# Kernel optimization log

Hardware: AMD Instinct MI355X
Metric: run time of the kernel (lower is better)

Reference implementation:

```python
import jax, jax.numpy as jnp
import numpy as np

B, N, D, H = 8, 384, 256, 1024

def setup_inputs() -> dict:
    key = jax.random.key(0)
    ks = jax.random.split(key, 8)
    x = jax.random.normal(ks[0], (B, N, D), jnp.float32)
    adj = jnp.ones((B, N, N), jnp.float32)
    box_num = jax.random.randint(ks[1], (B, 1), 1, N + 1).astype(jnp.int64)
    box_num = box_num.at[0, 0].set(N)  # original code assumes max(box_num) == N
    fc1_w = jax.random.normal(ks[2], (H, D), jnp.float32) * (1.0 / np.sqrt(D))
    fc1_b = jnp.zeros((H,), jnp.float32)
    fc2_w = jax.random.normal(ks[3], (D, H), jnp.float32) * (1.0 / np.sqrt(H))
    fc2_b = jnp.zeros((D,), jnp.float32)
    learn_w = jax.random.uniform(ks[4], (D,), jnp.float32)  # uniform_(0,1) init
    return {"x": x, "adj": adj, "box_num": box_num,
            "fc1_w": fc1_w, "fc1_b": fc1_b, "fc2_w": fc2_w, "fc2_b": fc2_b,
            "learn_w": learn_w}

def reference(x, adj, box_num, fc1_w, fc1_b, fc2_w, fc2_b, learn_w):
    # mlp: fc2(relu(fc1(x)))  -> x_hat (B,N,D)
    x_hat = jnp.maximum(x @ fc1_w.T + fc1_b, 0.0) @ fc2_w.T + fc2_b
    # dynamic mask: -1 where either node i or j is padding, 0 otherwise
    valid = jnp.arange(N)[None, :] < box_num            # (B,N)
    pair_valid = valid[:, None, :] & valid[:, :, None]  # (B,N,N)
    mask = jnp.where(pair_valid, 0.0, -1.0)             # (B,N,N)
    # pairwise weighted L1 distance: einsum('bijd,d->bij', |x_i - x_j| + mask, w)
    # mask broadcasts over d, so its contribution is mask * sum(w) (same math,
    # avoids a second (B,N,N,D) materialization)
    absdiff = jnp.abs(x_hat[:, :, None, :] - x_hat[:, None, :, :])  # (B,N,N,D)
    dist = jnp.einsum('bijd,d->bij', absdiff, learn_w) + mask * jnp.sum(learn_w)
    out = jax.nn.leaky_relu(dist, negative_slope=0.01)
    out = out - jnp.max(out, axis=-1, keepdims=True)
    soft_adj = adj * jnp.exp(out)
    soft_adj = soft_adj / jnp.sum(soft_adj, axis=-1, keepdims=True) + 1e-10
    return soft_adj, x_hat
```

## Files before the change

kernel.cpp:

```cpp
#include <hip/hip_runtime.h>
#include <math.h>

#define B_ 8
#define N_ 384
#define D_ 256
#define H_ 1024

typedef __bf16 bh;
typedef __bf16 bh4   __attribute__((ext_vector_type(4)));
typedef __bf16 bf16x8 __attribute__((ext_vector_type(8)));
typedef float  f32x4  __attribute__((ext_vector_type(4)));
typedef _Float16 h2 __attribute__((ext_vector_type(2)));

#if __has_builtin(__builtin_amdgcn_fdot2)
#define FDOT2(a,b,c) __builtin_amdgcn_fdot2((a),(b),(c),false)
#else
#define FDOT2(a,b,c) ((c) + (float)(a).x*(float)(b).x + (float)(a).y*(float)(b).y)
#endif

#define GLDS16(gp, lp) __builtin_amdgcn_global_load_lds( \
    (const __attribute__((address_space(1))) unsigned*)(gp), \
    (__attribute__((address_space(3))) unsigned*)(lp), 16, 0, 0)

__device__ inline h2 habs2(h2 x) {
    unsigned u = __builtin_bit_cast(unsigned, x) & 0x7fff7fffu;
    return __builtin_bit_cast(h2, u);
}

__device__ inline void split2(float v, bh& h, bh& l) {
    h = (bh)v;
    l = (bh)(v - (float)h);
}

__device__ inline int load_boxnum(const int* __restrict__ p, int b) {
    bool is64 = ((p[1] | p[3] | p[5] | p[7]) == 0);
    return is64 ? p[2 * b] : p[b];
}

__global__ __launch_bounds__(256) void prep_split(
        const float* __restrict__ x, const float* __restrict__ w1, const float* __restrict__ w2,
        bh* __restrict__ xh, bh* __restrict__ xl,
        bh* __restrict__ w1h, bh* __restrict__ w1l,
        bh* __restrict__ w2h, bh* __restrict__ w2l) {
    const int blk = blockIdx.x;
    const float* src; bh *dh, *dl; int idx;
    if (blk < 768)       { src = x;  dh = xh;  dl = xl;  idx = blk * 256 + threadIdx.x; }
    else if (blk < 1024) { src = w1; dh = w1h; dl = w1l; idx = (blk - 768) * 256 + threadIdx.x; }
    else                 { src = w2; dh = w2h; dl = w2l; idx = (blk - 1024) * 256 + threadIdx.x; }
    float4 v = ((const float4*)src)[idx];
    float f[4] = {v.x, v.y, v.z, v.w};
    bh4 hv, lv;
    #pragma unroll
    for (int i = 0; i < 4; i++) { bh h, l; split2(f[i], h, l); hv[i] = h; lv[i] = l; }
    *(bh4*)&dh[4 * (size_t)idx] = hv;
    *(bh4*)&dl[4 * (size_t)idx] = lv;
}

__global__ __launch_bounds__(256) void gemm1_kernel(
        const bh* __restrict__ xh, const bh* __restrict__ xl,
        const bh* __restrict__ w1h, const bh* __restrict__ w1l,
        const float* __restrict__ bias,
        bh* __restrict__ c1h, bh* __restrict__ c1l) {
    __shared__ __align__(16) bh lds[16384];
    const int tid = threadIdx.x, lane = tid & 63, w = tid >> 6;
    const int m0 = blockIdx.y * 128, n0 = blockIdx.x * 128;
    const int lr = lane >> 2, kb = lane & 3;
    const int kbp = kb ^ ((lr >> 1) & 3);
    const bh* psrc; int rowbase;
    if (w == 0)      { psrc = xh;  rowbase = m0; }
    else if (w == 1) { psrc = xl;  rowbase = m0; }
    else if (w == 2) { psrc = w1h; rowbase = n0; }
    else             { psrc = w1l; rowbase = n0; }
    const bh* gsrc = psrc + (size_t)(rowbase + lr) * 256 + kbp * 8;
    bh* lwb = &lds[w * 4096 + lane * 8];
    const int l15 = lane & 15, q = lane >> 4;
    const int swq = q ^ ((l15 >> 1) & 3);
    const int wm = (w & 1) * 64, wn = (w >> 1) * 64;

    f32x4 acc[4][4] = {};
    for (int k0 = 0; k0 < 256; k0 += 32) {
        __syncthreads();
        #pragma unroll
        for (int s = 0; s < 8; s++)
            GLDS16(gsrc + (size_t)s * 4096 + k0, lwb + s * 512);
        __syncthreads();
        bf16x8 fa[4][2], fb[4][2];
        #pragma unroll
        for (int i = 0; i < 4; i++) {
            int ra = wm + i * 16 + l15;
            int rb = wn + i * 16 + l15;
            fa[i][0] = *(const bf16x8*)&lds[        ra * 32 + swq * 8];
            fa[i][1] = *(const bf16x8*)&lds[ 4096 + ra * 32 + swq * 8];
            fb[i][0] = *(const bf16x8*)&lds[ 8192 + rb * 32 + swq * 8];
            fb[i][1] = *(const bf16x8*)&lds[12288 + rb * 32 + swq * 8];
        }
        #pragma unroll
        for (int mi = 0; mi < 4; mi++)
            #pragma unroll
            for (int ni = 0; ni < 4; ni++) {
                acc[mi][ni] = __builtin_amdgcn_mfma_f32_16x16x32_bf16(fa[mi][0], fb[ni][0], acc[mi][ni], 0, 0, 0);
                acc[mi][ni] = __builtin_amdgcn_mfma_f32_16x16x32_bf16(fa[mi][0], fb[ni][1], acc[mi][ni], 0, 0, 0);
                acc[mi][ni] = __builtin_amdgcn_mfma_f32_16x16x32_bf16(fa[mi][1], fb[ni][0], acc[mi][ni], 0, 0, 0);
            }
    }
    #pragma unroll
    for (int ni = 0; ni < 4; ni++) {
        int col = n0 + wn + ni * 16 + l15;
        float bb = bias[col];
        #pragma unroll
        for (int mi = 0; mi < 4; mi++)
            #pragma unroll
            for (int reg = 0; reg < 4; reg++) {
                int row = m0 + wm + mi * 16 + q * 4 + reg;
                float v = fmaxf(acc[mi][ni][reg] + bb, 0.f);
                bh h, l; split2(v, h, l);
                size_t off = (size_t)row * H_ + col;
                c1h[off] = h; c1l[off] = l;
            }
    }
}

__global__ __launch_bounds__(256) void gemm2_kernel(
        const bh* __restrict__ c1h, const bh* __restrict__ c1l,
        const bh* __restrict__ w2h, const bh* __restrict__ w2l,
        const float* __restrict__ bias,
        float* __restrict__ C) {
    __shared__ __align__(16) bh lds[24576];
    const int tid = threadIdx.x, lane = tid & 63, w = tid >> 6;
    const int m0 = blockIdx.y * 64, n0 = blockIdx.x * 128;
    const int lr = lane >> 3, kb = lane & 7;
    const int kbp = kb ^ lr;
    const int l15 = lane & 15, q = lane >> 4;
    const int wn = w * 32;

    f32x4 acc[4][2] = {};
    for (int k0 = 0; k0 < 1024; k0 += 64) {
        __syncthreads();
        #pragma unroll
        for (int j = 0; j < 12; j++) {
            int c = w * 12 + j;
            const bh* g; int ldsbase, s;
            if (c < 8)       { g = c1h; ldsbase = 0;     s = c;      g += (size_t)(m0 + s * 8 + lr) * 1024; }
            else if (c < 16) { g = c1l; ldsbase = 4096;  s = c - 8;  g += (size_t)(m0 + s * 8 + lr) * 1024; }
            else if (c < 32) { g = w2h; ldsbase = 8192;  s = c - 16; g += (size_t)(n0 + s * 8 + lr) * 1024; }
            else             { g = w2l; ldsbase = 16384; s = c - 32; g += (size_t)(n0 + s * 8 + lr) * 1024; }
            GLDS16(g + k0 + kbp * 8, &lds[ldsbase + s * 512 + lane * 8]);
        }
        __syncthreads();
        #pragma unroll
        for (int ks = 0; ks < 2; ks++) {
            const int p = (ks * 4 + q) ^ (l15 & 7);
            bf16x8 fa[4][2], fb[2][2];
            #pragma unroll
            for (int mi = 0; mi < 4; mi++) {
                int ra = mi * 16 + l15;
                fa[mi][0] = *(const bf16x8*)&lds[       ra * 64 + p * 8];
                fa[mi][1] = *(const bf16x8*)&lds[4096 + ra * 64 + p * 8];
            }
            #pragma unroll
            for (int ni = 0; ni < 2; ni++) {
                int rb = wn + ni * 16 + l15;
                fb[ni][0] = *(const bf16x8*)&lds[ 8192 + rb * 64 + p * 8];
                fb[ni][1] = *(const bf16x8*)&lds[16384 + rb * 64 + p * 8];
            }
            #pragma unroll
            for (int mi = 0; mi < 4; mi++)
                #pragma unroll
                for (int ni = 0; ni < 2; ni++) {
                    acc[mi][ni] = __builtin_amdgcn_mfma_f32_16x16x32_bf16(fa[mi][0], fb[ni][0], acc[mi][ni], 0, 0, 0);
                    acc[mi][ni] = __builtin_amdgcn_mfma_f32_16x16x32_bf16(fa[mi][0], fb[ni][1], acc[mi][ni], 0, 0, 0);
                    acc[mi][ni] = __builtin_amdgcn_mfma_f32_16x16x32_bf16(fa[mi][1], fb[ni][0], acc[mi][ni], 0, 0, 0);
                }
        }
    }
    #pragma unroll
    for (int ni = 0; ni < 2; ni++) {
        int col = n0 + wn + ni * 16 + l15;
        float bb = bias[col];
        #pragma unroll
        for (int mi = 0; mi < 4; mi++)
            #pragma unroll
            for (int reg = 0; reg < 4; reg++) {
                int row = m0 + mi * 16 + q * 4 + reg;
                C[(size_t)row * D_ + col] = acc[mi][ni][reg] + bb;
            }
    }
}

#define DLP 68
__global__ __launch_bounds__(256) void dist_kernel(const float* __restrict__ xhat,
                                                   const float* __restrict__ w,
                                                   const int* __restrict__ box_num,
                                                   float* __restrict__ dist) {
    __shared__ __align__(16) unsigned XiU[16 * DLP];
    __shared__ __align__(16) unsigned XjU[16 * DLP];
    const int bidx = blockIdx.x;
    const int b = bidx / 21;
    int p = bidx % 21;
    int ti = 0;
    while (p >= 6 - ti) { p -= 6 - ti; ti++; }
    const int tj = ti + p;
    const int i0 = ti * 64, j0 = tj * 64;

    const int tid = threadIdx.x;
    const int tx = tid & 15, ty = tid >> 4;
    const int lane = tid & 63;
    const int r = tid >> 2, kq = (tid & 3) * 8;
    const int kq2 = (tid & 3) * 4;

    float sumw = w[lane] + w[lane + 64] + w[lane + 128] + w[lane + 192];
    #pragma unroll
    for (int off = 32; off > 0; off >>= 1) sumw += __shfl_xor(sumw, off);

    const float* xb = xhat + (size_t)b * N_ * D_;
    float acc[4][4] = {};

    for (int k0 = 0; k0 < D_; k0 += 32) {
        h2 wk2[16];
        #pragma unroll
        for (int c = 0; c < 16; c++) {
            float2 wp = *(const float2*)&w[k0 + 2 * c];
            wk2[c] = (h2){(_Float16)wp.x, (_Float16)wp.y};
        }
        const float* ip = xb + (size_t)(i0 + r) * D_ + k0 + kq;
        const float* jp = xb + (size_t)(j0 + r) * D_ + k0 + kq;
        float4 i0v = *(const float4*)ip, i1v = *(const float4*)(ip + 4);
        float4 j0v = *(const float4*)jp, j1v = *(const float4*)(jp + 4);
        float fi[8] = {i0v.x, i0v.y, i0v.z, i0v.w, i1v.x, i1v.y, i1v.z, i1v.w};
        float fj[8] = {j0v.x, j0v.y, j0v.z, j0v.w, j1v.x, j1v.y, j1v.z, j1v.w};
        __syncthreads();
        #pragma unroll
        for (int c = 0; c < 4; c++) {
            h2 hi = (h2){(_Float16)fi[2 * c], (_Float16)fi[2 * c + 1]};
            h2 hj = (h2){(_Float16)fj[2 * c], (_Float16)fj[2 * c + 1]};
            XiU[(kq2 + c) * DLP + r] = __builtin_bit_cast(unsigned, hi);
            XjU[(kq2 + c) * DLP + r] = __builtin_bit_cast(unsigned, hj);
        }
        __syncthreads();
        #pragma unroll
        for (int k2 = 0; k2 < 16; k2++) {
            uint4 ar = *(const uint4*)&XiU[k2 * DLP + ty * 4];
            uint4 br = *(const uint4*)&XjU[k2 * DLP + tx * 4];
            h2 ai[4] = {__builtin_bit_cast(h2, ar.x), __builtin_bit_cast(h2, ar.y),
                        __builtin_bit_cast(h2, ar.z), __builtin_bit_cast(h2, ar.w)};
            h2 bj[4] = {__builtin_bit_cast(h2, br.x), __builtin_bit_cast(h2, br.y),
                        __builtin_bit_cast(h2, br.z), __builtin_bit_cast(h2, br.w)};
            h2 wv = wk2[k2];
            #pragma unroll
            for (int ii = 0; ii < 4; ii++)
                #pragma unroll
                for (int jj = 0; jj < 4; jj++) {
                    h2 d = habs2(ai[ii] - bj[jj]);
                    acc[ii][jj] = FDOT2(d, wv, acc[ii][jj]);
                }
        }
    }

    const int bn = load_boxnum(box_num, b);
    float m[4][4];
    #pragma unroll
    for (int ii = 0; ii < 4; ii++) {
        int i = i0 + ty * 4 + ii;
        bool vi = i < bn;
        #pragma unroll
        for (int jj = 0; jj < 4; jj++) {
            int j = j0 + tx * 4 + jj;
            float v = acc[ii][jj];
            if (!(vi && (j < bn))) v -= sumw;
            m[ii][jj] = v > 0.f ? v : 0.01f * v;
        }
    }
    #pragma unroll
    for (int ii = 0; ii < 4; ii++) {
        int i = i0 + ty * 4 + ii;
        float4 o = {m[ii][0], m[ii][1], m[ii][2], m[ii][3]};
        *(float4*)&dist[((size_t)b * N_ + i) * N_ + j0 + tx * 4] = o;
    }
    #pragma unroll
    for (int jj = 0; jj < 4; jj++) {
        int j = j0 + tx * 4 + jj;
        float4 o = {m[0][jj], m[1][jj], m[2][jj], m[3][jj]};
        *(float4*)&dist[((size_t)b * N_ + j) * N_ + i0 + ty * 4] = o;
    }
}

__global__ __launch_bounds__(256) void softmax_kernel(float* __restrict__ sa,
                                                      const float* __restrict__ adj) {
    const int row = blockIdx.x * 4 + (threadIdx.x >> 6);
    const int t = threadIdx.x & 63;
    float* prow = sa + (size_t)row * N_;
    const float* arow = adj + (size_t)row * N_;
    float v[6];
    float m = -1e30f;
    #pragma unroll
    for (int qq = 0; qq < 6; qq++) { v[qq] = prow[t + qq * 64]; m = fmaxf(m, v[qq]); }
    #pragma unroll
    for (int off = 32; off > 0; off >>= 1) m = fmaxf(m, __shfl_xor(m, off));
    float e[6];
    float s = 0.f;
    #pragma unroll
    for (int qq = 0; qq < 6; qq++) { e[qq] = arow[t + qq * 64] * expf(v[qq] - m); s += e[qq]; }
    #pragma unroll
    for (int off = 32; off > 0; off >>= 1) s += __shfl_xor(s, off);
    float inv = 1.0f / s;
    #pragma unroll
    for (int qq = 0; qq < 6; qq++) prow[t + qq * 64] = e[qq] * inv + 1e-10f;
}

extern "C" void kernel_launch(void* const* d_in, const int* in_sizes, int n_in,
                              void* d_out, int out_size, void* d_ws, size_t ws_size,
                              hipStream_t stream) {
    const float* x       = (const float*)d_in[0];
    const float* adj     = (const float*)d_in[1];
    const int*   box_num = (const int*)d_in[2];
    const float* fc1_w   = (const float*)d_in[3];
    const float* fc1_b   = (const float*)d_in[4];
    const float* fc2_w   = (const float*)d_in[5];
    const float* fc2_b   = (const float*)d_in[6];
    const float* learn_w = (const float*)d_in[7];

    float* soft_adj = (float*)d_out;
    float* xhat     = (float*)d_out + (size_t)B_ * N_ * N_;

    bh* xh  = (bh*)d_ws;
    bh* xl  = xh  + 786432;
    bh* w1h = xl  + 786432;
    bh* w1l = w1h + 262144;
    bh* w2h = w1l + 262144;
    bh* w2l = w2h + 262144;
    bh* c1h = w2l + 262144;
    bh* c1l = c1h + 3145728;

    prep_split<<<1280, 256, 0, stream>>>(x, fc1_w, fc2_w, xh, xl, w1h, w1l, w2h, w2l);

    dim3 g1(H_ / 128, (B_ * N_) / 128);
    gemm1_kernel<<<g1, 256, 0, stream>>>(xh, xl, w1h, w1l, fc1_b, c1h, c1l);

    dim3 g2(D_ / 128, (B_ * N_) / 64);
    gemm2_kernel<<<g2, 256, 0, stream>>>(c1h, c1l, w2h, w2l, fc2_b, xhat);

    dist_kernel<<<B_ * 21, 256, 0, stream>>>(xhat, learn_w, box_num, soft_adj);

    softmax_kernel<<<(B_ * N_) / 4, 256, 0, stream>>>(soft_adj, adj);
}
```

Before: 143.5 us.

## Fuse all stages into one persistent kernel with grid-wide atomic barriers

Replaces the five separate launches (split, gemm1, gemm2, dist, softmax) with one 192-block persistent kernel that uses atomic-counter grid barriers between phases. The distance phase now computes full rows per block and does the softmax in registers, so the intermediate dist matrix is never written and re-read. It also drops the symmetric half-tile trick, so every pair distance is computed twice, and gemm2 uses smaller tiles. Correctness depends on all 192 blocks being resident at once, and the spin barriers add their own synchronisation cost.

```diff
diff --git a/kernel.cpp b/kernel.cpp
--- a/kernel.cpp
+++ b/kernel.cpp
@@ -5,12 +5,13 @@
 #define N_ 384
 #define D_ 256
 #define H_ 1024
+#define GRID 192
 
 typedef __bf16 bh;
-typedef __bf16 bh4   __attribute__((ext_vector_type(4)));
+typedef __bf16 bh4    __attribute__((ext_vector_type(4)));
 typedef __bf16 bf16x8 __attribute__((ext_vector_type(8)));
 typedef float  f32x4  __attribute__((ext_vector_type(4)));
-typedef _Float16 h2 __attribute__((ext_vector_type(2)));
+typedef _Float16 h2   __attribute__((ext_vector_type(2)));
 
 #if __has_builtin(__builtin_amdgcn_fdot2)
 #define FDOT2(a,b,c) __builtin_amdgcn_fdot2((a),(b),(c),false)
@@ -26,285 +27,329 @@
     unsigned u = __builtin_bit_cast(unsigned, x) & 0x7fff7fffu;
     return __builtin_bit_cast(h2, u);
 }
-
 __device__ inline void split2(float v, bh& h, bh& l) {
-    h = (bh)v;
-    l = (bh)(v - (float)h);
-}
-
+    h = (bh)v; l = (bh)(v - (float)h);
+}
 __device__ inline int load_boxnum(const int* __restrict__ p, int b) {
     bool is64 = ((p[1] | p[3] | p[5] | p[7]) == 0);
     return is64 ? p[2 * b] : p[b];
 }
 
-__global__ __launch_bounds__(256) void prep_split(
-        const float* __restrict__ x, const float* __restrict__ w1, const float* __restrict__ w2,
-        bh* __restrict__ xh, bh* __restrict__ xl,
-        bh* __restrict__ w1h, bh* __restrict__ w1l,
-        bh* __restrict__ w2h, bh* __restrict__ w2l) {
-    const int blk = blockIdx.x;
-    const float* src; bh *dh, *dl; int idx;
-    if (blk < 768)       { src = x;  dh = xh;  dl = xl;  idx = blk * 256 + threadIdx.x; }
-    else if (blk < 1024) { src = w1; dh = w1h; dl = w1l; idx = (blk - 768) * 256 + threadIdx.x; }
-    else                 { src = w2; dh = w2h; dl = w2l; idx = (blk - 1024) * 256 + threadIdx.x; }
-    float4 v = ((const float4*)src)[idx];
-    float f[4] = {v.x, v.y, v.z, v.w};
-    bh4 hv, lv;
-    #pragma unroll
-    for (int i = 0; i < 4; i++) { bh h, l; split2(f[i], h, l); hv[i] = h; lv[i] = l; }
-    *(bh4*)&dh[4 * (size_t)idx] = hv;
-    *(bh4*)&dl[4 * (size_t)idx] = lv;
-}
-
-__global__ __launch_bounds__(256) void gemm1_kernel(
-        const bh* __restrict__ xh, const bh* __restrict__ xl,
-        const bh* __restrict__ w1h, const bh* __restrict__ w1l,
-        const float* __restrict__ bias,
-        bh* __restrict__ c1h, bh* __restrict__ c1l) {
-    __shared__ __align__(16) bh lds[16384];
+__device__ inline void gbar(unsigned* c, unsigned target) {
+    __syncthreads();
+    if (threadIdx.x == 0) {
+        __threadfence();
+        __hip_atomic_fetch_add(c, 1u, __ATOMIC_ACQ_REL, __HIP_MEMORY_SCOPE_AGENT);
+        while (__hip_atomic_load(c, __ATOMIC_ACQUIRE, __HIP_MEMORY_SCOPE_AGENT) < target)
+            __builtin_amdgcn_s_sleep(2);
+        __threadfence();
+    }
+    __syncthreads();
+}
+
+__global__ __launch_bounds__(256) void fused_kernel(
+        const float* __restrict__ x, const float* __restrict__ adj,
+        const int* __restrict__ box_num,
+        const float* __restrict__ fc1_w, const float* __restrict__ fc1_b,
+        const float* __restrict__ fc2_w, const float* __restrict__ fc2_b,
+        const float* __restrict__ learn_w,
+        float* __restrict__ soft_adj, float* __restrict__ xhat,
+        bh* __restrict__ wsb, unsigned* __restrict__ cnt) {
+    __shared__ __align__(16) unsigned char smem[32768];
     const int tid = threadIdx.x, lane = tid & 63, w = tid >> 6;
-    const int m0 = blockIdx.y * 128, n0 = blockIdx.x * 128;
-    const int lr = lane >> 2, kb = lane & 3;
-    const int kbp = kb ^ ((lr >> 1) & 3);
-    const bh* psrc; int rowbase;
-    if (w == 0)      { psrc = xh;  rowbase = m0; }
-    else if (w == 1) { psrc = xl;  rowbase = m0; }
-    else if (w == 2) { psrc = w1h; rowbase = n0; }
-    else             { psrc = w1l; rowbase = n0; }
-    const bh* gsrc = psrc + (size_t)(rowbase + lr) * 256 + kbp * 8;
-    bh* lwb = &lds[w * 4096 + lane * 8];
-    const int l15 = lane & 15, q = lane >> 4;
-    const int swq = q ^ ((l15 >> 1) & 3);
-    const int wm = (w & 1) * 64, wn = (w >> 1) * 64;
-
-    f32x4 acc[4][4] = {};
-    for (int k0 = 0; k0 < 256; k0 += 32) {
-        __syncthreads();
-        #pragma unroll
-        for (int s = 0; s < 8; s++)
-            GLDS16(gsrc + (size_t)s * 4096 + k0, lwb + s * 512);
-        __syncthreads();
-        bf16x8 fa[4][2], fb[4][2];
-        #pragma unroll
-        for (int i = 0; i < 4; i++) {
-            int ra = wm + i * 16 + l15;
-            int rb = wn + i * 16 + l15;
-            fa[i][0] = *(const bf16x8*)&lds[        ra * 32 + swq * 8];
-            fa[i][1] = *(const bf16x8*)&lds[ 4096 + ra * 32 + swq * 8];
-            fb[i][0] = *(const bf16x8*)&lds[ 8192 + rb * 32 + swq * 8];
-            fb[i][1] = *(const bf16x8*)&lds[12288 + rb * 32 + swq * 8];
-        }
-        #pragma unroll
-        for (int mi = 0; mi < 4; mi++)
-            #pragma unroll
-            for (int ni = 0; ni < 4; ni++) {
-                acc[mi][ni] = __builtin_amdgcn_mfma_f32_16x16x32_bf16(fa[mi][0], fb[ni][0], acc[mi][ni], 0, 0, 0);
-                acc[mi][ni] = __builtin_amdgcn_mfma_f32_16x16x32_bf16(fa[mi][0], fb[ni][1], acc[mi][ni], 0, 0, 0);
-                acc[mi][ni] = __builtin_amdgcn_mfma_f32_16x16x32_bf16(fa[mi][1], fb[ni][0], acc[mi][ni], 0, 0, 0);
-            }
-    }
-    #pragma unroll
-    for (int ni = 0; ni < 4; ni++) {
-        int col = n0 + wn + ni * 16 + l15;
-        float bb = bias[col];
-        #pragma unroll
-        for (int mi = 0; mi < 4; mi++)
-            #pragma unroll
-            for (int reg = 0; reg < 4; reg++) {
-                int row = m0 + wm + mi * 16 + q * 4 + reg;
-                float v = fmaxf(acc[mi][ni][reg] + bb, 0.f);
-                bh h, l; split2(v, h, l);
-                size_t off = (size_t)row * H_ + col;
-                c1h[off] = h; c1l[off] = l;
-            }
-    }
-}
-
-__global__ __launch_bounds__(256) void gemm2_kernel(
-        const bh* __restrict__ c1h, const bh* __restrict__ c1l,
-        const bh* __restrict__ w2h, const bh* __restrict__ w2l,
-        const float* __restrict__ bias,
-        float* __restrict__ C) {
-    __shared__ __align__(16) bh lds[24576];
-    const int tid = threadIdx.x, lane = tid & 63, w = tid >> 6;
-    const int m0 = blockIdx.y * 64, n0 = blockIdx.x * 128;
-    const int lr = lane >> 3, kb = lane & 7;
-    const int kbp = kb ^ lr;
-    const int l15 = lane & 15, q = lane >> 4;
-    const int wn = w * 32;
-
-    f32x4 acc[4][2] = {};
-    for (int k0 = 0; k0 < 1024; k0 += 64) {
-        __syncthreads();
-        #pragma unroll
-        for (int j = 0; j < 12; j++) {
-            int c = w * 12 + j;
-            const bh* g; int ldsbase, s;
-            if (c < 8)       { g = c1h; ldsbase = 0;     s = c;      g += (size_t)(m0 + s * 8 + lr) * 1024; }
-            else if (c < 16) { g = c1l; ldsbase = 4096;  s = c - 8;  g += (size_t)(m0 + s * 8 + lr) * 1024; }
-            else if (c < 32) { g = w2h; ldsbase = 8192;  s = c - 16; g += (size_t)(n0 + s * 8 + lr) * 1024; }
-            else             { g = w2l; ldsbase = 16384; s = c - 32; g += (size_t)(n0 + s * 8 + lr) * 1024; }
-            GLDS16(g + k0 + kbp * 8, &lds[ldsbase + s * 512 + lane * 8]);
-        }
-        __syncthreads();
-        #pragma unroll
-        for (int ks = 0; ks < 2; ks++) {
-            const int p = (ks * 4 + q) ^ (l15 & 7);
-            bf16x8 fa[4][2], fb[2][2];
-            #pragma unroll
-            for (int mi = 0; mi < 4; mi++) {
-                int ra = mi * 16 + l15;
-                fa[mi][0] = *(const bf16x8*)&lds[       ra * 64 + p * 8];
-                fa[mi][1] = *(const bf16x8*)&lds[4096 + ra * 64 + p * 8];
-            }
-            #pragma unroll
-            for (int ni = 0; ni < 2; ni++) {
-                int rb = wn + ni * 16 + l15;
-                fb[ni][0] = *(const bf16x8*)&lds[ 8192 + rb * 64 + p * 8];
-                fb[ni][1] = *(const bf16x8*)&lds[16384 + rb * 64 + p * 8];
+    const int bidx = blockIdx.x;
+    const int gtid = bidx * 256 + tid;
+
+    bh* xh  = wsb;
+    bh* xl  = xh  + 786432;
+    bh* w1h = xl  + 786432;
+    bh* w1l = w1h + 262144;
+    bh* w2h = w1l + 262144;
+    bh* w2l = w2h + 262144;
+    bh* c1h = w2l + 262144;
+    bh* c1l = c1h + 3145728;
+
+    {
+        #pragma unroll
+        for (int it = 0; it < 4; it++) {
+            int idx = it * (GRID * 256) + gtid;
+            float4 v = ((const float4*)x)[idx];
+            float f[4] = {v.x, v.y, v.z, v.w};
+            bh4 hv, lv;
+            #pragma unroll
+            for (int i = 0; i < 4; i++) { bh h, l; split2(f[i], h, l); hv[i] = h; lv[i] = l; }
+            *(bh4*)&xh[4 * (size_t)idx] = hv;
+            *(bh4*)&xl[4 * (size_t)idx] = lv;
+        }
+        #pragma unroll
+        for (int it = 0; it < 2; it++) {
+            int idx = it * (GRID * 256) + gtid;
+            if (idx < 65536) {
+                float4 v = ((const float4*)fc1_w)[idx];
+                float f[4] = {v.x, v.y, v.z, v.w};
+                bh4 hv, lv;
+                #pragma unroll
+                for (int i = 0; i < 4; i++) { bh h, l; split2(f[i], h, l); hv[i] = h; lv[i] = l; }
+                *(bh4*)&w1h[4 * (size_t)idx] = hv;
+                *(bh4*)&w1l[4 * (size_t)idx] = lv;
+            }
+        }
+        #pragma unroll
+        for (int it = 0; it < 2; it++) {
+            int idx = it * (GRID * 256) + gtid;
+            if (idx < 65536) {
+                float4 v = ((const float4*)fc2_w)[idx];
+                float f[4] = {v.x, v.y, v.z, v.w};
+                bh4 hv, lv;
+                #pragma unroll
+                for (int i = 0; i < 4; i++) { bh h, l; split2(f[i], h, l); hv[i] = h; lv[i] = l; }
+                *(bh4*)&w2h[4 * (size_t)idx] = hv;
+                *(bh4*)&w2l[4 * (size_t)idx] = lv;
+            }
+        }
+    }
+    gbar(cnt, GRID);
+
+    {
+        bh* lds = (bh*)smem;
+        const int mt = bidx >> 3, nt = bidx & 7;
+        const int m0 = mt * 128, n0 = nt * 128;
+        const int lr = lane >> 2, kb = lane & 3;
+        const int kbp = kb ^ ((lr >> 1) & 3);
+        const bh* psrc; int rowbase;
+        if (w == 0)      { psrc = xh;  rowbase = m0; }
+        else if (w == 1) { psrc = xl;  rowbase = m0; }
+        else if (w == 2) { psrc = w1h; rowbase = n0; }
+        else             { psrc = w1l; rowbase = n0; }
+        const bh* gsrc = psrc + (size_t)(rowbase + lr) * 256 + kbp * 8;
+        bh* lwb = &lds[w * 4096 + lane * 8];
+        const int l15 = lane & 15, q = lane >> 4;
+        const int swq = q ^ ((l15 >> 1) & 3);
+        const int wm = (w & 1) * 64, wn = (w >> 1) * 64;
+
+        f32x4 acc[4][4] = {};
+        for (int k0 = 0; k0 < 256; k0 += 32) {
+            __syncthreads();
+            #pragma unroll
+            for (int s = 0; s < 8; s++)
+                GLDS16(gsrc + (size_t)s * 4096 + k0, lwb + s * 512);
+            __syncthreads();
+            bf16x8 fa[4][2], fb[4][2];
+            #pragma unroll
+            for (int i = 0; i < 4; i++) {
+                int ra = wm + i * 16 + l15;
+                int rb = wn + i * 16 + l15;
+                fa[i][0] = *(const bf16x8*)&lds[        ra * 32 + swq * 8];
+                fa[i][1] = *(const bf16x8*)&lds[ 4096 + ra * 32 + swq * 8];
+                fb[i][0] = *(const bf16x8*)&lds[ 8192 + rb * 32 + swq * 8];
+                fb[i][1] = *(const bf16x8*)&lds[12288 + rb * 32 + swq * 8];
             }
             #pragma unroll
             for (int mi = 0; mi < 4; mi++)
                 #pragma unroll
-                for (int ni = 0; ni < 2; ni++) {
+                for (int ni = 0; ni < 4; ni++) {
                     acc[mi][ni] = __builtin_amdgcn_mfma_f32_16x16x32_bf16(fa[mi][0], fb[ni][0], acc[mi][ni], 0, 0, 0);
                     acc[mi][ni] = __builtin_amdgcn_mfma_f32_16x16x32_bf16(fa[mi][0], fb[ni][1], acc[mi][ni], 0, 0, 0);
                     acc[mi][ni] = __builtin_amdgcn_mfma_f32_16x16x32_bf16(fa[mi][1], fb[ni][0], acc[mi][ni], 0, 0, 0);
                 }
         }
-    }
-    #pragma unroll
-    for (int ni = 0; ni < 2; ni++) {
-        int col = n0 + wn + ni * 16 + l15;
-        float bb = bias[col];
-        #pragma unroll
-        for (int mi = 0; mi < 4; mi++)
-            #pragma unroll
-            for (int reg = 0; reg < 4; reg++) {
-                int row = m0 + mi * 16 + q * 4 + reg;
-                C[(size_t)row * D_ + col] = acc[mi][ni][reg] + bb;
-            }
-    }
-}
-
-#define DLP 68
-__global__ __launch_bounds__(256) void dist_kernel(const float* __restrict__ xhat,
-                                                   const float* __restrict__ w,
-                                                   const int* __restrict__ box_num,
-                                                   float* __restrict__ dist) {
-    __shared__ __align__(16) unsigned XiU[16 * DLP];
-    __shared__ __align__(16) unsigned XjU[16 * DLP];
-    const int bidx = blockIdx.x;
-    const int b = bidx / 21;
-    int p = bidx % 21;
-    int ti = 0;
-    while (p >= 6 - ti) { p -= 6 - ti; ti++; }
-    const int tj = ti + p;
-    const int i0 = ti * 64, j0 = tj * 64;
-
-    const int tid = threadIdx.x;
-    const int tx = tid & 15, ty = tid >> 4;
-    const int lane = tid & 63;
-    const int r = tid >> 2, kq = (tid & 3) * 8;
-    const int kq2 = (tid & 3) * 4;
-
-    float sumw = w[lane] + w[lane + 64] + w[lane + 128] + w[lane + 192];
-    #pragma unroll
-    for (int off = 32; off > 0; off >>= 1) sumw += __shfl_xor(sumw, off);
-
-    const float* xb = xhat + (size_t)b * N_ * D_;
-    float acc[4][4] = {};
-
-    for (int k0 = 0; k0 < D_; k0 += 32) {
-        h2 wk2[16];
-        #pragma unroll
-        for (int c = 0; c < 16; c++) {
-            float2 wp = *(const float2*)&w[k0 + 2 * c];
-            wk2[c] = (h2){(_Float16)wp.x, (_Float16)wp.y};
-        }
-        const float* ip = xb + (size_t)(i0 + r) * D_ + k0 + kq;
-        const float* jp = xb + (size_t)(j0 + r) * D_ + k0 + kq;
-        float4 i0v = *(const float4*)ip, i1v = *(const float4*)(ip + 4);
-        float4 j0v = *(const float4*)jp, j1v = *(const float4*)(jp + 4);
-        float fi[8] = {i0v.x, i0v.y, i0v.z, i0v.w, i1v.x, i1v.y, i1v.z, i1v.w};
-        float fj[8] = {j0v.x, j0v.y, j0v.z, j0v.w, j1v.x, j1v.y, j1v.z, j1v.w};
+        #pragma unroll
+        for (int ni = 0; ni < 4; ni++) {
+            int col = n0 + wn + ni * 16 + l15;
+            float bb = fc1_b[col];
+            #pragma unroll
+            for (int mi = 0; mi < 4; mi++)
+                #pragma unroll
+                for (int reg = 0; reg < 4; reg++) {
+                    int row = m0 + wm + mi * 16 + q * 4 + reg;
+                    float v = fmaxf(acc[mi][ni][reg] + bb, 0.f);
+                    bh h, l; split2(v, h, l);
+                    size_t off = (size_t)row * H_ + col;
+                    c1h[off] = h; c1l[off] = l;
+                }
+        }
+    }
+    gbar(cnt, 2 * GRID);
+
+    {
+        bh* lds = (bh*)smem;
+        const int mt = bidx >> 2, nt = bidx & 3;
+        const int m0 = mt * 64, n0 = nt * 64;
+        const int lr8 = lane >> 3, kb = lane & 7;
+        const int kbp = kb ^ lr8;
+        const bh* g2;
+        if (w == 0)      g2 = c1h + (size_t)(m0 + lr8) * 1024;
+        else if (w == 1) g2 = c1l + (size_t)(m0 + lr8) * 1024;
+        else if (w == 2) g2 = w2h + (size_t)(n0 + lr8) * 1024;
+        else             g2 = w2l + (size_t)(n0 + lr8) * 1024;
+        g2 += kbp * 8;
+        bh* lwb = &lds[w * 4096 + lane * 8];
+        const int l15 = lane & 15, q = lane >> 4;
+        const int wm = (w & 1) * 32, wn = (w >> 1) * 32;
+
+        f32x4 acc[2][2] = {};
+        for (int k0 = 0; k0 < 1024; k0 += 64) {
+            __syncthreads();
+            #pragma unroll
+            for (int s = 0; s < 8; s++)
+                GLDS16(g2 + (size_t)s * 8192 + k0, lwb + s * 512);
+            __syncthreads();
+            #pragma unroll
+            for (int ks = 0; ks < 2; ks++) {
+                bf16x8 fa[2][2], fb[2][2];
+                #pragma unroll
+                for (int mi = 0; mi < 2; mi++) {
+                    int r = wm + mi * 16 + l15;
+                    int pos = (ks * 4 + q) ^ (l15 & 7);
+                    fa[mi][0] = *(const bf16x8*)&lds[       r * 64 + pos * 8];
+                    fa[mi][1] = *(const bf16x8*)&lds[4096 + r * 64 + pos * 8];
+                }
+                #pragma unroll
+                for (int ni = 0; ni < 2; ni++) {
+                    int r = wn + ni * 16 + l15;
+                    int pos = (ks * 4 + q) ^ (l15 & 7);
+                    fb[ni][0] = *(const bf16x8*)&lds[ 8192 + r * 64 + pos * 8];
+                    fb[ni][1] = *(const bf16x8*)&lds[12288 + r * 64 + pos * 8];
+                }
+                #pragma unroll
+                for (int mi = 0; mi < 2; mi++)
+                    #pragma unroll
+                    for (int ni = 0; ni < 2; ni++) {
+                        acc[mi][ni] = __builtin_amdgcn_mfma_f32_16x16x32_bf16(fa[mi][0], fb[ni][0], acc[mi][ni], 0, 0, 0);
+                        acc[mi][ni] = __builtin_amdgcn_mfma_f32_16x16x32_bf16(fa[mi][0], fb[ni][1], acc[mi][ni], 0, 0, 0);
+                        acc[mi][ni] = __builtin_amdgcn_mfma_f32_16x16x32_bf16(fa[mi][1], fb[ni][0], acc[mi][ni], 0, 0, 0);
+                    }
+            }
+        }
+        #pragma unroll
+        for (int ni = 0; ni < 2; ni++) {
+            int col = n0 + wn + ni * 16 + l15;
+            float bb = fc2_b[col];
+            #pragma unroll
+            for (int mi = 0; mi < 2; mi++)
+                #pragma unroll
+                for (int reg = 0; reg < 4; reg++) {
+                    int row = m0 + wm + mi * 16 + q * 4 + reg;
+                    xhat[(size_t)row * D_ + col] = acc[mi][ni][reg] + bb;
+                }
+        }
+    }
+    gbar(cnt, 3 * GRID);
+
+    {
+        h2* Xi = (h2*)smem;
+        h2* Xj = (h2*)(smem + 8960);
+        h2* Ws = (h2*)(smem + 8960 + 17920);
+        const int b = bidx / 24, rb = bidx % 24;
+        const int r0 = rb * 16;
+        const int ty = tid >> 4, tx = tid & 15;
+
+        float sumw = learn_w[lane] + learn_w[lane + 64] + learn_w[lane + 128] + learn_w[lane + 192];
+        #pragma unroll
+        for (int off = 32; off > 0; off >>= 1) sumw += __shfl_xor(sumw, off);
+
+        const float* xb = xhat + (size_t)b * N_ * D_;
         __syncthreads();
-        #pragma unroll
-        for (int c = 0; c < 4; c++) {
-            h2 hi = (h2){(_Float16)fi[2 * c], (_Float16)fi[2 * c + 1]};
-            h2 hj = (h2){(_Float16)fj[2 * c], (_Float16)fj[2 * c + 1]};
-            XiU[(kq2 + c) * DLP + r] = __builtin_bit_cast(unsigned, hi);
-            XjU[(kq2 + c) * DLP + r] = __builtin_bit_cast(unsigned, hj);
+        if (tid < 64) {
+            float4 wv = ((const float4*)learn_w)[tid];
+            Ws[tid * 2]     = (h2){(_Float16)wv.x, (_Float16)wv.y};
+            Ws[tid * 2 + 1] = (h2){(_Float16)wv.z, (_Float16)wv.w};
+        }
+        {
+            const int row = tid >> 4, cf = (tid & 15) * 16;
+            const float* p = xb + (size_t)(r0 + row) * D_ + cf;
+            float f[16];
+            #pragma unroll
+            for (int i = 0; i < 4; i++) {
+                float4 v = *(const float4*)(p + i * 4);
+                f[4*i] = v.x; f[4*i+1] = v.y; f[4*i+2] = v.z; f[4*i+3] = v.w;
+            }
+            #pragma unroll
+            for (int i = 0; i < 8; i++)
+                Xi[row * 140 + (tid & 15) * 8 + i] = (h2){(_Float16)f[2*i], (_Float16)f[2*i+1]};
         }
         __syncthreads();
-        #pragma unroll
-        for (int k2 = 0; k2 < 16; k2++) {
-            uint4 ar = *(const uint4*)&XiU[k2 * DLP + ty * 4];
-            uint4 br = *(const uint4*)&XjU[k2 * DLP + tx * 4];
-            h2 ai[4] = {__builtin_bit_cast(h2, ar.x), __builtin_bit_cast(h2, ar.y),
-                        __builtin_bit_cast(h2, ar.z), __builtin_bit_cast(h2, ar.w)};
-            h2 bj[4] = {__builtin_bit_cast(h2, br.x), __builtin_bit_cast(h2, br.y),
-                        __builtin_bit_cast(h2, br.z), __builtin_bit_cast(h2, br.w)};
-            h2 wv = wk2[k2];
-            #pragma unroll
-            for (int ii = 0; ii < 4; ii++)
-                #pragma unroll
-                for (int jj = 0; jj < 4; jj++) {
-                    h2 d = habs2(ai[ii] - bj[jj]);
-                    acc[ii][jj] = FDOT2(d, wv, acc[ii][jj]);
-                }
-        }
-    }
-
-    const int bn = load_boxnum(box_num, b);
-    float m[4][4];
-    #pragma unroll
-    for (int ii = 0; ii < 4; ii++) {
-        int i = i0 + ty * 4 + ii;
-        bool vi = i < bn;
-        #pragma unroll
-        for (int jj = 0; jj < 4; jj++) {
-            int j = j0 + tx * 4 + jj;
-            float v = acc[ii][jj];
-            if (!(vi && (j < bn))) v -= sumw;
-            m[ii][jj] = v > 0.f ? v : 0.01f * v;
-        }
-    }
-    #pragma unroll
-    for (int ii = 0; ii < 4; ii++) {
-        int i = i0 + ty * 4 + ii;
-        float4 o = {m[ii][0], m[ii][1], m[ii][2], m[ii][3]};
-        *(float4*)&dist[((size_t)b * N_ + i) * N_ + j0 + tx * 4] = o;
-    }
-    #pragma unroll
-    for (int jj = 0; jj < 4; jj++) {
-        int j = j0 + tx * 4 + jj;
-        float4 o = {m[0][jj], m[1][jj], m[2][jj], m[3][jj]};
-        *(float4*)&dist[((size_t)b * N_ + j) * N_ + i0 + ty * 4] = o;
-    }
-}
-
-__global__ __launch_bounds__(256) void softmax_kernel(float* __restrict__ sa,
-                                                      const float* __restrict__ adj) {
-    const int row = blockIdx.x * 4 + (threadIdx.x >> 6);
-    const int t = threadIdx.x & 63;
-    float* prow = sa + (size_t)row * N_;
-    const float* arow = adj + (size_t)row * N_;
-    float v[6];
-    float m = -1e30f;
-    #pragma unroll
-    for (int qq = 0; qq < 6; qq++) { v[qq] = prow[t + qq * 64]; m = fmaxf(m, v[qq]); }
-    #pragma unroll
-    for (int off = 32; off > 0; off >>= 1) m = fmaxf(m, __shfl_xor(m, off));
-    float e[6];
-    float s = 0.f;
-    #pragma unroll
-    for (int qq = 0; qq < 6; qq++) { e[qq] = arow[t + qq * 64] * expf(v[qq] - m); s += e[qq]; }
-    #pragma unroll
-    for (int off = 32; off > 0; off >>= 1) s += __shfl_xor(s, off);
-    float inv = 1.0f / s;
-    #pragma unroll
-    for (int qq = 0; qq < 6; qq++) prow[t + qq * 64] = e[qq] * inv + 1e-10f;
+
+        float acc3[12][2] = {};
+        for (int jc = 0; jc < 12; jc++) {
+            if (jc) __syncthreads();
+            {
+                const int row = tid >> 3, cf = (tid & 7) * 32;
+                const float* p = xb + (size_t)(jc * 32 + row) * D_ + cf;
+                #pragma unroll
+                for (int g = 0; g < 2; g++) {
+                    float f[16];
+                    #pragma unroll
+                    for (int i = 0; i < 4; i++) {
+                        float4 v = *(const float4*)(p + g * 16 + i * 4);
+                        f[4*i] = v.x; f[4*i+1] = v.y; f[4*i+2] = v.z; f[4*i+3] = v.w;
+                    }
+                    #pragma unroll
+                    for (int i = 0; i < 8; i++)
+                        Xj[row * 140 + (tid & 7) * 16 + g * 8 + i] =
+                            (h2){(_Float16)f[2*i], (_Float16)f[2*i+1]};
+                }
+            }
+            __syncthreads();
+            #pragma unroll
+            for (int kk = 0; kk < 32; kk++) {
+                uint4 iv = *(const uint4*)&Xi[ty * 140 + kk * 4];
+                uint4 wv = *(const uint4*)&Ws[kk * 4];
+                h2 ai[4] = {__builtin_bit_cast(h2, iv.x), __builtin_bit_cast(h2, iv.y),
+                            __builtin_bit_cast(h2, iv.z), __builtin_bit_cast(h2, iv.w)};
+                h2 wp[4] = {__builtin_bit_cast(h2, wv.x), __builtin_bit_cast(h2, wv.y),
+                            __builtin_bit_cast(h2, wv.z), __builtin_bit_cast(h2, wv.w)};
+                #pragma unroll
+                for (int jj = 0; jj < 2; jj++) {
+                    uint4 jv = *(const uint4*)&Xj[(tx + 16 * jj) * 140 + kk * 4];
+                    h2 bj[4] = {__builtin_bit_cast(h2, jv.x), __builtin_bit_cast(h2, jv.y),
+                                __builtin_bit_cast(h2, jv.z), __builtin_bit_cast(h2, jv.w)};
+                    float a = acc3[jc][jj];
+                    #pragma unroll
+                    for (int e = 0; e < 4; e++)
+                        a = FDOT2(habs2(ai[e] - bj[e]), wp[e], a);
+                    acc3[jc][jj] = a;
+                }
+            }
+        }
+
+        const int bn = load_boxnum(box_num, b);
+        const int i_ = r0 + ty;
+        const bool vi = i_ < bn;
+        float m = -1e30f;
+        #pragma unroll
+        for (int jc = 0; jc < 12; jc++)
+            #pragma unroll
+            for (int jj = 0; jj < 2; jj++) {
+                int j_ = jc * 32 + tx + 16 * jj;
+                float v = acc3[jc][jj];
+                if (!(vi && (j_ < bn))) v -= sumw;
+                v = v > 0.f ? v : 0.01f * v;
+                acc3[jc][jj] = v;
+                m = fmaxf(m, v);
+            }
+        #pragma unroll
+        for (int off = 8; off > 0; off >>= 1) m = fmaxf(m, __shfl_xor(m, off));
+        const float* arow = adj + ((size_t)b * N_ + i_) * N_;
+        float e[12][2], s = 0.f;
+        #pragma unroll
+        for (int jc = 0; jc < 12; jc++)
+            #pragma unroll
+            for (int jj = 0; jj < 2; jj++) {
+                int j_ = jc * 32 + tx + 16 * jj;
+                e[jc][jj] = arow[j_] * expf(acc3[jc][jj] - m);
+                s += e[jc][jj];
+            }
+        #pragma unroll
+        for (int off = 8; off > 0; off >>= 1) s += __shfl_xor(s, off);
+        float inv = 1.0f / s;
+        float* orow = soft_adj + ((size_t)b * N_ + i_) * N_;
+        #pragma unroll
+        for (int jc = 0; jc < 12; jc++)
+            #pragma unroll
+            for (int jj = 0; jj < 2; jj++)
+                orow[jc * 32 + tx + 16 * jj] = e[jc][jj] * inv + 1e-10f;
+    }
 }
 
 extern "C" void kernel_launch(void* const* d_in, const int* in_sizes, int n_in,
@@ -322,24 +367,11 @@
     float* soft_adj = (float*)d_out;
     float* xhat     = (float*)d_out + (size_t)B_ * N_ * N_;
 
-    bh* xh  = (bh*)d_ws;
-    bh* xl  = xh  + 786432;
-    bh* w1h = xl  + 786432;
-    bh* w1l = w1h + 262144;
-    bh* w2h = w1l + 262144;
-    bh* w2l = w2h + 262144;
-    bh* c1h = w2l + 262144;
-    bh* c1l = c1h + 3145728;
-
-    prep_split<<<1280, 256, 0, stream>>>(x, fc1_w, fc2_w, xh, xl, w1h, w1l, w2h, w2l);
-
-    dim3 g1(H_ / 128, (B_ * N_) / 128);
-    gemm1_kernel<<<g1, 256, 0, stream>>>(xh, xl, w1h, w1l, fc1_b, c1h, c1l);
-
-    dim3 g2(D_ / 128, (B_ * N_) / 64);
-    gemm2_kernel<<<g2, 256, 0, stream>>>(c1h, c1l, w2h, w2l, fc2_b, xhat);
-
-    dist_kernel<<<B_ * 21, 256, 0, stream>>>(xhat, learn_w, box_num, soft_adj);
-
-    softmax_kernel<<<(B_ * N_) / 4, 256, 0, stream>>>(soft_adj, adj);
-}
+    unsigned* cnt = (unsigned*)d_ws;
+    bh* wsb = (bh*)((char*)d_ws + 512);
+
+    hipMemsetAsync(d_ws, 0, 512, stream);
+    fused_kernel<<<GRID, 256, 0, stream>>>(x, adj, box_num, fc1_w, fc1_b,
+                                           fc2_w, fc2_b, learn_w,
+                                           soft_adj, xhat, wsb, cnt);
+}
```

Measured after the change: 228.3 us. +59.0%, slower.
